# Optimization experiments

Measured on AMD Instinct MI355X. Metric: run time of the kernel, lower is better.

## Reference

```python
import jax, jax.numpy as jnp
import numpy as np

B, C, H, W = 2, 128, 64, 64
N, R = 16, 4            # d_state, dt_rank = ceil(128/32)
R2 = 2 * R
Ch = C // 2
Cout = 128
L = H * W
EPS_LN = 1e-6
EPS_BN = 1e-5


def _ln_cf(x, w, b):
    # channels_first LayerNorm over dim 1
    u = x.mean(1, keepdims=True)
    s = ((x - u) ** 2).mean(1, keepdims=True)
    return w[None, :, None, None] * (x - u) / jnp.sqrt(s + EPS_LN) + b[None, :, None, None]


def _conv1x1(x, w, b):
    return jnp.einsum('bchw,oc->bohw', x, w) + b[None, :, None, None]


def _dwconv(x, w, b):
    out = jax.lax.conv_general_dilated(x, w, (1, 1), 'SAME',
        dimension_numbers=('NCHW', 'OIHW', 'NCHW'), feature_group_count=x.shape[1])
    return out + b[None, :, None, None]


def _selective_scan(u, delta, A, Bs, Cs, D):
    # u, delta: [B,L,C]; A: [C,N]; Bs, Cs: [B,L,N]; D: [C]
    dA = jnp.exp(delta[..., None] * A)                   # [B,L,C,N]
    dBu = (delta * u)[..., None] * Bs[:, :, None, :]     # [B,L,C,N]
    def step(h, xs):
        a, b = xs
        h = a * h + b
        return h, h
    h0 = jnp.zeros((u.shape[0], u.shape[2], A.shape[1]), u.dtype)
    _, hs = jax.lax.scan(step, h0, (jnp.moveaxis(dA, 1, 0), jnp.moveaxis(dBu, 1, 0)))
    hs = jnp.moveaxis(hs, 0, 1)                          # [B,L,C,N]
    return jnp.einsum('blcn,bln->blc', hs, Cs) + u * D


def _branch_ssm(x, xp_w, xp_b, dt_w, dt_b, A_log, Dp, reverse):
    b_, c_, h_, w_ = x.shape
    u = x.reshape(b_, c_, -1).transpose(0, 2, 1)         # [B,L,C/2]
    if reverse:
        u = u[:, ::-1]
    dbl = u @ xp_w.T + xp_b
    dt, Bs, Cs = jnp.split(dbl, [R, R + N], axis=-1)
    delta = jax.nn.softplus(dt @ dt_w.T + dt_b)
    y = _selective_scan(u, delta, -jnp.exp(A_log), Bs, Cs, Dp)
    if reverse:
        y = y[:, ::-1]
    return y.transpose(0, 2, 1).reshape(b_, c_, h_, w_)


def _sid_ssm(x, sorted_idx, xp_w, xp_b, dt_w, dt_b, A_log, Dp):
    b_, c_, h_, w_ = x.shape
    u = x.reshape(b_, c_, -1).transpose(0, 2, 1)         # [B,L,C]
    u = jnp.take_along_axis(u, sorted_idx[:, :, None], axis=1)
    dbl = u @ xp_w.T + xp_b
    dt, Bs, Cs = jnp.split(dbl, [R2, R2 + N], axis=-1)
    delta = jax.nn.softplus(dt @ dt_w.T + dt_b)
    y = _selective_scan(u, delta, -jnp.exp(A_log), Bs, Cs, Dp)
    inv = jnp.argsort(sorted_idx, axis=1)                # inverse permutation
    y = jnp.take_along_axis(y, inv[:, :, None], axis=1)
    return y.transpose(0, 2, 1).reshape(b_, c_, h_, w_)


def _forward(x, mask_fg, mask_bg, mask_uc,
             norm_in_w, norm_in_b, in_proj_w, in_proj_b,
             ln_mamba_w, ln_mamba_b, conv_mamba_w, conv_mamba_b,
             conv_res_w, conv_res_b,
             xproj_f_w, xproj_f_b, dtproj_f_w, dtproj_f_b, A_log_f, D_f,
             xproj_b_w, xproj_b_b, dtproj_b_w, dtproj_b_b, A_log_b, D_b,
             xproj_s_w, xproj_s_b, dtproj_s_w, dtproj_s_b, A_log_s, D_s,
             ln_cat_w, ln_cat_b,
             g0_w, g0_b, bn_g, bn_be, bn_m, bn_v, g1_w, g1_b,
             out_w, out_b, norm_out_w, norm_out_b):
    x = _ln_cf(x, norm_in_w, norm_in_b)
    xp = _conv1x1(x, in_proj_w, in_proj_b)               # [B,2C,H,W]
    x_mamba, x_res = xp[:, :C], xp[:, C:]
    x_mamba = _ln_cf(x_mamba, ln_mamba_w, ln_mamba_b)
    x_mamba = jax.nn.silu(_dwconv(x_mamba, conv_mamba_w, conv_mamba_b))
    x_res = jax.nn.silu(_dwconv(x_res, conv_res_w, conv_res_b))
    xf, xb = x_mamba[:, :Ch], x_mamba[:, Ch:]
    y_f = _branch_ssm(xf, xproj_f_w, xproj_f_b, dtproj_f_w, dtproj_f_b, A_log_f, D_f, False)
    y_b = _branch_ssm(xb, xproj_b_w, xproj_b_b, dtproj_b_w, dtproj_b_b, A_log_b, D_b, True)
    concat = _ln_cf(jnp.concatenate([y_f, y_b], 1), ln_cat_w, ln_cat_b)
    # SID priority ordering: fg > bg > uc > rest, ties broken by raster index
    fg = (mask_fg > 0.5).astype(x.dtype)
    bg = (mask_bg > 0.5).astype(x.dtype) * (1 - fg)
    uc = (mask_uc > 0.5).astype(x.dtype) * (1 - fg) * (1 - bg)
    prio = (fg * 3 + bg * 2 + uc).reshape(x.shape[0], -1) \
        + jnp.arange(L, dtype=x.dtype)[None] * 1e-4
    sorted_idx = jnp.argsort(-prio, axis=1)
    sid = _sid_ssm(x_mamba, sorted_idx, xproj_s_w, xproj_s_b, dtproj_s_w, dtproj_s_b, A_log_s, D_s)
    # gated fusion (BatchNorm in eval mode with running stats)
    g = _conv1x1(jnp.concatenate([concat, sid], 1), g0_w, g0_b)
    g = (g - bn_m[None, :, None, None]) / jnp.sqrt(bn_v + EPS_BN)[None, :, None, None]
    g = jax.nn.relu(g * bn_g[None, :, None, None] + bn_be[None, :, None, None])
    g = jax.nn.sigmoid(_conv1x1(g, g1_w, g1_b))
    fused = g * sid + (1 - g) * concat
    out = _conv1x1(jnp.concatenate([fused, x_res], 1), out_w, out_b)
    return _ln_cf(out, norm_out_w, norm_out_b)


def setup_inputs():
    keys = iter(jax.random.split(jax.random.key(0), 64))
    def rn(shape, s=1.0):
        return jax.random.normal(next(keys), shape, jnp.float32) * s
    def dt_bias(ch):
        dt = jnp.exp(jax.random.uniform(next(keys), (ch,)) * (np.log(0.1) - np.log(0.001)) + np.log(0.001))
        return dt + jnp.log(-jnp.expm1(-dt))  # inverse-softplus init as in torch code
    def a_log(ch):
        return jnp.log(jnp.tile(jnp.arange(1, N + 1, dtype=jnp.float32), (ch, 1)))
    s = 0.05
    return dict(
        x=rn((B, C, H, W)),
        mask_fg=jax.random.uniform(next(keys), (B, 1, H, W)),
        mask_bg=jax.random.uniform(next(keys), (B, 1, H, W)),
        mask_uc=jax.random.uniform(next(keys), (B, 1, H, W)),
        norm_in_w=jnp.ones((C,)), norm_in_b=jnp.zeros((C,)),
        in_proj_w=rn((2 * C, C), s), in_proj_b=jnp.zeros((2 * C,)),
        ln_mamba_w=jnp.ones((C,)), ln_mamba_b=jnp.zeros((C,)),
        conv_mamba_w=rn((C, 1, 3, 3), 0.2), conv_mamba_b=jnp.zeros((C,)),
        conv_res_w=rn((C, 1, 3, 3), 0.2), conv_res_b=jnp.zeros((C,)),
        xproj_f_w=rn((R + 2 * N, Ch), s), xproj_f_b=jnp.zeros((R + 2 * N,)),
        dtproj_f_w=rn((Ch, R), 0.5), dtproj_f_b=dt_bias(Ch),
        A_log_f=a_log(Ch), D_f=jnp.ones((Ch,)),
        xproj_b_w=rn((R + 2 * N, Ch), s), xproj_b_b=jnp.zeros((R + 2 * N,)),
        dtproj_b_w=rn((Ch, R), 0.5), dtproj_b_b=dt_bias(Ch),
        A_log_b=a_log(Ch), D_b=jnp.ones((Ch,)),
        xproj_s_w=rn((R2 + 2 * N, C), s), xproj_s_b=jnp.zeros((R2 + 2 * N,)),
        dtproj_s_w=rn((C, R2), 0.35), dtproj_s_b=dt_bias(C),
        A_log_s=a_log(C), D_s=jnp.ones((C,)),
        ln_cat_w=jnp.ones((C,)), ln_cat_b=jnp.zeros((C,)),
        g0_w=rn((C, 2 * C), s), g0_b=jnp.zeros((C,)),
        bn_g=jnp.ones((C,)), bn_be=jnp.zeros((C,)),
        bn_m=jnp.zeros((C,)), bn_v=jnp.ones((C,)),
        g1_w=rn((C, C), s), g1_b=jnp.zeros((C,)),
        out_w=rn((Cout, 2 * C), s), out_b=jnp.zeros((Cout,)),
        norm_out_w=jnp.ones((Cout,)), norm_out_b=jnp.zeros((Cout,)),
    )


def reference(x, mask_fg, mask_bg, mask_uc,
              norm_in_w, norm_in_b, in_proj_w, in_proj_b,
              ln_mamba_w, ln_mamba_b, conv_mamba_w, conv_mamba_b,
              conv_res_w, conv_res_b,
              xproj_f_w, xproj_f_b, dtproj_f_w, dtproj_f_b, A_log_f, D_f,
              xproj_b_w, xproj_b_b, dtproj_b_w, dtproj_b_b, A_log_b, D_b,
              xproj_s_w, xproj_s_b, dtproj_s_w, dtproj_s_b, A_log_s, D_s,
              ln_cat_w, ln_cat_b,
              g0_w, g0_b, bn_g, bn_be, bn_m, bn_v, g1_w, g1_b,
              out_w, out_b, norm_out_w, norm_out_b):
    return _forward(x, mask_fg, mask_bg, mask_uc,
                    norm_in_w, norm_in_b, in_proj_w, in_proj_b,
                    ln_mamba_w, ln_mamba_b, conv_mamba_w, conv_mamba_b,
                    conv_res_w, conv_res_b,
                    xproj_f_w, xproj_f_b, dtproj_f_w, dtproj_f_b, A_log_f, D_f,
                    xproj_b_w, xproj_b_b, dtproj_b_w, dtproj_b_b, A_log_b, D_b,
                    xproj_s_w, xproj_s_b, dtproj_s_w, dtproj_s_b, A_log_s, D_s,
                    ln_cat_w, ln_cat_b,
                    g0_w, g0_b, bn_g, bn_be, bn_m, bn_v, g1_w, g1_b,
                    out_w, out_b, norm_out_w, norm_out_b)
```

## Files before the change

### kernel.cpp

```cpp
#include <hip/hip_runtime.h>
#include <math.h>

#define Bn 2
#define Cn_ 128
#define Hn 64
#define Wn 64
#define Ln 4096
#define Nn 16

static constexpr float EPS_LN_C = 1e-6f;
static constexpr float EPS_BN_C = 1e-5f;

__device__ __forceinline__ float softplusf_(float x) {
    return fmaxf(x, 0.f) + log1pf(__expf(-fabsf(x)));
}
__device__ __forceinline__ float sigmoidf_(float x) {
    return 1.f / (1.f + __expf(-x));
}

__global__ __launch_bounds__(256) void ln_kernel(
    const float* __restrict__ inA, const float* __restrict__ inB, int csA,
    const float* __restrict__ lw, const float* __restrict__ lb,
    float* __restrict__ out, int csOut) {
    int b = blockIdx.y;
// ... 101 lines not shown
        for (int j = 0; j < 4; j++) {
            int o = o0 + j;
            if (o >= cout) continue;
            float4 v = acc[j];
            if (epilogue == 1) {
                float sc = (1.f / sqrtf(bnv[o] + EPS_BN_C)) * bng[o];
                float sh = bnbe[o] - bnm[o] * sc;
                v.x = fmaxf(fmaf(v.x, sc, sh), 0.f);
                v.y = fmaxf(fmaf(v.y, sc, sh), 0.f);
                v.z = fmaxf(fmaf(v.z, sc, sh), 0.f);
                v.w = fmaxf(fmaf(v.w, sc, sh), 0.f);
            } else if (epilogue == 2) {
                v.x = sigmoidf_(v.x); v.y = sigmoidf_(v.y);
                v.z = sigmoidf_(v.z); v.w = sigmoidf_(v.w);
            }
            *(float4*)(out + ((size_t)b * csOut + o) * Ln + l) = v;
        }
    }
}

__global__ __launch_bounds__(256) void combine_kernel(
    const float* __restrict__ p0, const float* __restrict__ p1,
    const float* __restrict__ p2, const float* __restrict__ p3, int ksn,
    const float* __restrict__ bias,
    const float* __restrict__ bng, const float* __restrict__ bnbe,
    const float* __restrict__ bnm, const float* __restrict__ bnv,
    int epilogue, float* __restrict__ out, int cout, int n4) {
    int i = blockIdx.x * 256 + threadIdx.x;
    if (i >= n4) return;
    size_t e = (size_t)i * 4;
    int o = (int)((e / Ln) % cout);
    float4 a = *(const float4*)(p0 + e);
    if (ksn > 1) { float4 t = *(const float4*)(p1 + e); a.x += t.x; a.y += t.y; a.z += t.z; a.w += t.w; }
    if (ksn > 2) { float4 t = *(const float4*)(p2 + e); a.x += t.x; a.y += t.y; a.z += t.z; a.w += t.w; }
    if (ksn > 3) { float4 t = *(const float4*)(p3 + e); a.x += t.x; a.y += t.y; a.z += t.z; a.w += t.w; }
    float bj = bias[o];
    a.x += bj; a.y += bj; a.z += bj; a.w += bj;
    if (epilogue == 1) {
        float sc = (1.f / sqrtf(bnv[o] + EPS_BN_C)) * bng[o];
        float sh = bnbe[o] - bnm[o] * sc;
        a.x = fmaxf(fmaf(a.x, sc, sh), 0.f);
        a.y = fmaxf(fmaf(a.y, sc, sh), 0.f);
        a.z = fmaxf(fmaf(a.z, sc, sh), 0.f);
        a.w = fmaxf(fmaf(a.w, sc, sh), 0.f);
    } else if (epilogue == 2) {
        a.x = sigmoidf_(a.x); a.y = sigmoidf_(a.y);
        a.z = sigmoidf_(a.z); a.w = sigmoidf_(a.w);
    }
    *(float4*)(out + e) = a;
}

__global__ void dwconv_kernel(const float* __restrict__ xmn, const float* __restrict__ xp,
                              const float* __restrict__ wm, const float* __restrict__ bm,
                              const float* __restrict__ wr, const float* __restrict__ brr,
                              float* __restrict__ xm, float* __restrict__ xr) {
    int b = blockIdx.z;
    int c2 = blockIdx.y;
    int l = blockIdx.x * blockDim.x + threadIdx.x;
    int h = l >> 6, w = l & 63;
    bool mamba = (c2 < 128);
    const float* in = mamba ? (xmn + ((size_t)b * 128 + c2) * Ln)
                            : (xp + ((size_t)b * 256 + c2) * Ln);
    const float* wt = mamba ? (wm + c2 * 9) : (wr + (c2 - 128) * 9);
    float acc = mamba ? bm[c2] : brr[c2 - 128];
#pragma unroll
    for (int dh = -1; dh <= 1; dh++) {
#pragma unroll
        for (int dw = -1; dw <= 1; dw++) {
            int hh = h + dh, ww = w + dw;
            if (hh < 0 || hh > 63 || ww < 0 || ww > 63) continue;
            acc = fmaf(in[hh * 64 + ww], wt[(dh + 1) * 3 + (dw + 1)], acc);
        }
    }
    float o = acc * sigmoidf_(acc);
    if (mamba) xm[((size_t)b * 128 + c2) * Ln + l] = o;
    else       xr[((size_t)b * 128 + (c2 - 128)) * Ln + l] = o;
}

__global__ __launch_bounds__(1024) void sort_kernel(const float* __restrict__ mfg,
                                                    const float* __restrict__ mbg,
// ... 89 lines not shown
#pragma unroll
    for (int r = 0; r < R; r++) {
        float wv = dtw[c * R + r];
        acc.x = fmaf(wv, a[r].x, acc.x);
        acc.y = fmaf(wv, a[r].y, acc.y);
        acc.z = fmaf(wv, a[r].z, acc.z);
        acc.w = fmaf(wv, a[r].w, acc.w);
    }
    float4 o;
    o.x = softplusf_(acc.x); o.y = softplusf_(acc.y);
    o.z = softplusf_(acc.z); o.w = softplusf_(acc.w);
    *(float4*)(dpk + (((size_t)b * NQ + cq) * 1024 + tq) * 16 + clow * 4) = o;
}

__global__ __launch_bounds__(256) void pack_bc_kernel(
    const float* __restrict__ dblf, const float* __restrict__ dblb, const float* __restrict__ dbls,
    float* __restrict__ bf, float* __restrict__ cf,
    float* __restrict__ bb2, float* __restrict__ cb2,
    float* __restrict__ bs, float* __restrict__ cs) {
    int br = blockIdx.z;
    int b = blockIdx.y;
    int idx = blockIdx.x * 256 + threadIdx.x;
    int tb = idx >> 4, n = idx & 15;
    const float* src; float* dB; float* dC; int RT, rB, rC;
    if (br == 0)      { src = dblf; dB = bf;  dC = cf;  RT = 36; rB = 4; rC = 20; }
    else if (br == 1) { src = dblb; dB = bb2; dC = cb2; RT = 36; rB = 4; rC = 20; }
    else              { src = dbls; dB = bs;  dC = cs;  RT = 40; rB = 8; rC = 24; }
    float4 vB = *(const float4*)(src + ((size_t)b * RT + rB + n) * Ln + tb * 4);
    float4 vC = *(const float4*)(src + ((size_t)b * RT + rC + n) * Ln + tb * 4);
    *(float4*)(dB + ((size_t)b * 1024 + tb) * 64 + n * 4) = vB;
    *(float4*)(dC + ((size_t)b * 1024 + tb) * 64 + n * 4) = vC;
}

#define NCHUNK 64
#define CG 4

#define DPPADD(p) do { \
    p += __int_as_float(__builtin_amdgcn_update_dpp(0, __float_as_int(p), 0xB1, 0xF, 0xF, true)); \
    p += __int_as_float(__builtin_amdgcn_update_dpp(0, __float_as_int(p), 0x4E, 0xF, 0xF, true)); \
    p += __int_as_float(__builtin_amdgcn_update_dpp(0, __float_as_int(p), 0x124, 0xF, 0xF, true)); \
    p += __int_as_float(__builtin_amdgcn_update_dpp(0, __float_as_int(p), 0x128, 0xF, 0xF, true)); \
} while (0)

template <int REV>
__device__ __forceinline__ void p1_chunk(const float* __restrict__ up, const float* __restrict__ dp,
                                         const float* __restrict__ bp, float A, int c0,
                                         float& hout, float& Pout) {
    float h = 0.f, P = 1.f;
    float4 U0[4], D0[4], B0[4], U1[4], D1[4], B1[4];
#define PHYS1(ci) (REV ? (255 - (ci)) : (ci))
#define LOAD1(U, D, Bb, ci) do { int pb_ = PHYS1(ci) * 16; int tb_ = PHYS1(ci) * 4; \
    _Pragma("unroll") for (int j_ = 0; j_ < 4; ++j_) { \
        U[j_]  = *(const float4*)(up + pb_ + 4 * j_); \
        D[j_]  = *(const float4*)(dp + (size_t)(tb_ + j_) * 16); \
        Bb[j_] = *(const float4*)(bp + (size_t)(tb_ + j_) * 64); \
    } } while (0)
#define STEP1(u_, d_, B_) do { float a_ = __expf((d_) * A); h = fmaf(a_, h, (d_) * (u_) * (B_)); P *= a_; } while (0)
#define COMP1(U, D, Bb) do { \
    if (!REV) { _Pragma("unroll") for (int j_ = 0; j_ < 4; ++j_) { \
        STEP1(U[j_].x, D[j_].x, Bb[j_].x); STEP1(U[j_].y, D[j_].y, Bb[j_].y); \
        STEP1(U[j_].z, D[j_].z, Bb[j_].z); STEP1(U[j_].w, D[j_].w, Bb[j_].w); } } \
    else { _Pragma("unroll") for (int j_ = 3; j_ >= 0; --j_) { \
        STEP1(U[j_].w, D[j_].w, Bb[j_].w); STEP1(U[j_].z, D[j_].z, Bb[j_].z); \
        STEP1(U[j_].y, D[j_].y, Bb[j_].y); STEP1(U[j_].x, D[j_].x, Bb[j_].x); } } } while (0)
    LOAD1(U0, D0, B0, c0);
    for (int it = 0; it < CG; it += 2) {
        LOAD1(U1, D1, B1, c0 + it + 1);
        COMP1(U0, D0, B0);
        if (it + 2 < CG) LOAD1(U0, D0, B0, c0 + it + 2);
        COMP1(U1, D1, B1);
    }
    hout = h; Pout = P;
#undef PHYS1
#undef LOAD1
#undef STEP1
#undef COMP1
}

__global__ __launch_bounds__(256) void scan_p1_kernel(
    const float* __restrict__ xm, const float* __restrict__ us,
    const float* __restrict__ dfpk, const float* __restrict__ bpkf, const float* __restrict__ Alf,
    const float* __restrict__ dbpk, const float* __restrict__ bpkb, const float* __restrict__ Alb,
    const float* __restrict__ dspk, const float* __restrict__ bpks, const float* __restrict__ Als,
    float* __restrict__ hf, float* __restrict__ Pp) {
    int g = blockIdx.x * 4 + (threadIdx.x >> 6), k = blockIdx.y;
    int lane = threadIdx.x & 63;
    int n = lane & 15, cl = lane >> 4;
    int c0 = k * CG;
    float h, P;
    if (g < 32) {
        int b = g >> 4, cg = g & 15, c = cg * 4 + cl;
        float A = -__expf(Alf[c * 16 + n]);
        p1_chunk<0>(xm + ((size_t)b * 128 + c) * Ln,
                    dfpk + (((size_t)b * 16 + cg) * 1024) * 16 + cl * 4,
                    bpkf + (size_t)b * 65536 + n * 4, A, c0, h, P);
    } else if (g < 64) {
        int g2 = g - 32, b = g2 >> 4, cg = g2 & 15, c = cg * 4 + cl;
        float A = -__expf(Alb[c * 16 + n]);
        p1_chunk<1>(xm + ((size_t)b * 128 + 64 + c) * Ln,
                    dbpk + (((size_t)b * 16 + cg) * 1024) * 16 + cl * 4,
                    bpkb + (size_t)b * 65536 + n * 4, A, c0, h, P);
    } else {
        int g2 = g - 64, b = g2 >> 5, cg = g2 & 31, c = cg * 4 + cl;
        float A = -__expf(Als[c * 16 + n]);
        p1_chunk<0>(us + ((size_t)b * 128 + c) * Ln,
                    dspk + (((size_t)b * 32 + cg) * 1024) * 16 + cl * 4,
                    bpks + (size_t)b * 65536 + n * 4, A, c0, h, P);
    }
    int o = (g * NCHUNK + k) * 64 + lane;
    hf[o] = h; Pp[o] = P;
}

__global__ void scan_stitch_kernel(const float* __restrict__ hf, const float* __restrict__ Pp,
                                   float* __restrict__ hi) {
    int id = blockIdx.x * blockDim.x + threadIdx.x;
    int g = id >> 6, lane = id & 63;
    float h = 0.f;
    for (int kb = 0; kb < NCHUNK / 8; kb++) {
        float P8[8], H8[8];
#pragma unroll
        for (int j = 0; j < 8; j++) {
            int o = (g * NCHUNK + kb * 8 + j) * 64 + lane;
            P8[j] = Pp[o]; H8[j] = hf[o];
        }
#pragma unroll
        for (int j = 0; j < 8; j++) {
            int o = (g * NCHUNK + kb * 8 + j) * 64 + lane;
            hi[o] = h;
            h = fmaf(P8[j], h, H8[j]);
        }
    }
}

#define STEPP(u_, d_, B_, C_) ({ \
    float dA_ = __expf((d_) * A); \
    h = fmaf(dA_, h, (d_) * (u_) * (B_)); \
    float p_ = h * (C_); \
    DPPADD(p_); \
    fmaf((u_), Dc, p_); })

template <int MODE>
__device__ __forceinline__ void p2_chunk(const float* __restrict__ up, const float* __restrict__ dp,
                                         const float* __restrict__ bp, const float* __restrict__ cp,
                                         const int* __restrict__ sp, float* __restrict__ yp,
                                         float A, float Dc, int n, int c0, float h) {
    constexpr bool REV = (MODE == 1);
    constexpr bool SIDM = (MODE == 2);
    float4 U0[4], D0[4], B0[4], C0[4], U1[4], D1[4], B1[4], C1[4];
    int4 I0[4] = {}, I1[4] = {};
#define PHYS(ci) (REV ? (255 - (ci)) : (ci))
#define LOADC(U, D, Bb, Cc, I, ci) do { int pb_ = PHYS(ci) * 16; int tb_ = PHYS(ci) * 4; \
    _Pragma("unroll") for (int j_ = 0; j_ < 4; ++j_) { \
        U[j_]  = *(const float4*)(up + pb_ + 4 * j_); \
        D[j_]  = *(const float4*)(dp + (size_t)(tb_ + j_) * 16); \
        Bb[j_] = *(const float4*)(bp + (size_t)(tb_ + j_) * 64); \
        Cc[j_] = *(const float4*)(cp + (size_t)(tb_ + j_) * 64); \
        if (SIDM) I[j_] = *(const int4*)(sp + pb_ + 4 * j_); \
    } } while (0)
#define COMPC(U, D, Bb, Cc, I, ci) do { int pb_ = PHYS(ci) * 16; \
    if (SIDM) { \
        _Pragma("unroll") for (int j_ = 0; j_ < 4; ++j_) { \
            float y0_ = STEPP(U[j_].x, D[j_].x, Bb[j_].x, Cc[j_].x); if (n == 0) yp[I[j_].x] = y0_; \
            float y1_ = STEPP(U[j_].y, D[j_].y, Bb[j_].y, Cc[j_].y); if (n == 0) yp[I[j_].y] = y1_; \
            float y2_ = STEPP(U[j_].z, D[j_].z, Bb[j_].z, Cc[j_].z); if (n == 0) yp[I[j_].z] = y2_; \
            float y3_ = STEPP(U[j_].w, D[j_].w, Bb[j_].w, Cc[j_].w); if (n == 0) yp[I[j_].w] = y3_; \
        } \
    } else if (!REV) { \
        _Pragma("unroll") for (int j_ = 0; j_ < 4; ++j_) { \
            float4 y4_; \
            y4_.x = STEPP(U[j_].x, D[j_].x, Bb[j_].x, Cc[j_].x); \
            y4_.y = STEPP(U[j_].y, D[j_].y, Bb[j_].y, Cc[j_].y); \
            y4_.z = STEPP(U[j_].z, D[j_].z, Bb[j_].z, Cc[j_].z); \
            y4_.w = STEPP(U[j_].w, D[j_].w, Bb[j_].w, Cc[j_].w); \
            if (n == 0) *(float4*)(yp + pb_ + 4 * j_) = y4_; \
        } \
    } else { \
        _Pragma("unroll") for (int j_ = 3; j_ >= 0; --j_) { \
            float4 y4_; \
            y4_.w = STEPP(U[j_].w, D[j_].w, Bb[j_].w, Cc[j_].w); \
            y4_.z = STEPP(U[j_].z, D[j_].z, Bb[j_].z, Cc[j_].z); \
            y4_.y = STEPP(U[j_].y, D[j_].y, Bb[j_].y, Cc[j_].y); \
            y4_.x = STEPP(U[j_].x, D[j_].x, Bb[j_].x, Cc[j_].x); \
            if (n == 0) *(float4*)(yp + pb_ + 4 * j_) = y4_; \
        } \
    } } while (0)
    LOADC(U0, D0, B0, C0, I0, c0);
    for (int it = 0; it < CG; it += 2) {
        LOADC(U1, D1, B1, C1, I1, c0 + it + 1);
        COMPC(U0, D0, B0, C0, I0, c0 + it);
        if (it + 2 < CG) LOADC(U0, D0, B0, C0, I0, c0 + it + 2);
        COMPC(U1, D1, B1, C1, I1, c0 + it + 1);
    }
#undef PHYS
#undef LOADC
#undef COMPC
}

__global__ __launch_bounds__(256) void scan_p2_kernel(
    const float* __restrict__ xm, const float* __restrict__ us,
    const float* __restrict__ dfpk, const float* __restrict__ bpkf, const float* __restrict__ cpkf,
    const float* __restrict__ Alf, const float* __restrict__ Dfp,
    const float* __restrict__ dbpk, const float* __restrict__ bpkb, const float* __restrict__ cpkb,
    const float* __restrict__ Alb, const float* __restrict__ Dbp,
    const float* __restrict__ dspk, const float* __restrict__ bpks, const float* __restrict__ cpks,
    const float* __restrict__ Als, const float* __restrict__ Dsp,
    const int* __restrict__ sidx, const float* __restrict__ hi,
    float* __restrict__ yf, float* __restrict__ yb, float* __restrict__ ys) {
    int g = blockIdx.x * 4 + (threadIdx.x >> 6), k = blockIdx.y;
    int lane = threadIdx.x & 63;
    int n = lane & 15, cl = lane >> 4;
    int c0 = k * CG;
    float h0 = hi[(g * NCHUNK + k) * 64 + lane];
    if (g < 32) {
        int b = g >> 4, cg = g & 15, c = cg * 4 + cl;
        float A = -__expf(Alf[c * 16 + n]);
        p2_chunk<0>(xm + ((size_t)b * 128 + c) * Ln,
                    dfpk + (((size_t)b * 16 + cg) * 1024) * 16 + cl * 4,
                    bpkf + (size_t)b * 65536 + n * 4, cpkf + (size_t)b * 65536 + n * 4,
                    nullptr, yf + ((size_t)b * 64 + c) * Ln, A, Dfp[c], n, c0, h0);
    } else if (g < 64) {
        int g2 = g - 32, b = g2 >> 4, cg = g2 & 15, c = cg * 4 + cl;
        float A = -__expf(Alb[c * 16 + n]);
        p2_chunk<1>(xm + ((size_t)b * 128 + 64 + c) * Ln,
                    dbpk + (((size_t)b * 16 + cg) * 1024) * 16 + cl * 4,
                    bpkb + (size_t)b * 65536 + n * 4, cpkb + (size_t)b * 65536 + n * 4,
                    nullptr, yb + ((size_t)b * 64 + c) * Ln, A, Dbp[c], n, c0, h0);
    } else {
        int g2 = g - 64, b = g2 >> 5, cg = g2 & 31, c = cg * 4 + cl;
        float A = -__expf(Als[c * 16 + n]);
        p2_chunk<2>(us + ((size_t)b * 128 + c) * Ln,
                    dspk + (((size_t)b * 32 + cg) * 1024) * 16 + cl * 4,
                    bpks + (size_t)b * 65536 + n * 4, cpks + (size_t)b * 65536 + n * 4,
                    sidx + b * Ln, ys + ((size_t)b * 128 + c) * Ln, A, Dsp[c], n, c0, h0);
    }
}

__global__ void fuse_kernel(const float4* __restrict__ gate, const float4* __restrict__ ysb,
                            const float4* __restrict__ cat, float4* __restrict__ out, int n4) {
    int i = blockIdx.x * blockDim.x + threadIdx.x;
    if (i < n4) {
        float4 g = gate[i], s = ysb[i], c = cat[i], o;
        o.x = g.x * s.x + (1.f - g.x) * c.x;
        o.y = g.y * s.y + (1.f - g.y) * c.y;
        o.z = g.z * s.z + (1.f - g.z) * c.z;
        o.w = g.w * s.w + (1.f - g.w) * c.w;
        out[i] = o;
    }
}

extern "C" void kernel_launch(void* const* d_in, const int* in_sizes, int n_in,
                              void* d_out, int out_size, void* d_ws, size_t ws_size,
                              hipStream_t stream) {
    const float* x    = (const float*)d_in[0];
    const float* mfg  = (const float*)d_in[1];
    const float* mbg  = (const float*)d_in[2];
    const float* muc  = (const float*)d_in[3];
    const float* niw  = (const float*)d_in[4];
    const float* nib  = (const float*)d_in[5];
    const float* inw  = (const float*)d_in[6];
    const float* inb  = (const float*)d_in[7];
    const float* lmw  = (const float*)d_in[8];
    const float* lmb  = (const float*)d_in[9];
    const float* cmw  = (const float*)d_in[10];
    const float* cmb  = (const float*)d_in[11];
    const float* crw  = (const float*)d_in[12];
    const float* crb  = (const float*)d_in[13];
    const float* xwf  = (const float*)d_in[14];
    const float* xbf  = (const float*)d_in[15];
    const float* dtwf = (const float*)d_in[16];
    const float* dtbf = (const float*)d_in[17];
    const float* Alf  = (const float*)d_in[18];
    const float* Dfp  = (const float*)d_in[19];
    const float* xwb  = (const float*)d_in[20];
    const float* xbb  = (const float*)d_in[21];
    const float* dtwb = (const float*)d_in[22];
    const float* dtbb = (const float*)d_in[23];
    const float* Alb  = (const float*)d_in[24];
    const float* Dbp  = (const float*)d_in[25];
    const float* xws  = (const float*)d_in[26];
// ... 3 lines not shown
    const float* Als  = (const float*)d_in[30];
    const float* Dsp  = (const float*)d_in[31];
    const float* lcw  = (const float*)d_in[32];
    const float* lcb  = (const float*)d_in[33];
    const float* g0w  = (const float*)d_in[34];
    const float* g0b  = (const float*)d_in[35];
    const float* bng  = (const float*)d_in[36];
    const float* bnbe = (const float*)d_in[37];
    const float* bnm  = (const float*)d_in[38];
    const float* bnv  = (const float*)d_in[39];
    const float* g1w  = (const float*)d_in[40];
    const float* g1b  = (const float*)d_in[41];
    const float* outw = (const float*)d_in[42];
    const float* outb = (const float*)d_in[43];
    const float* now  = (const float*)d_in[44];
    const float* nob  = (const float*)d_in[45];

    float* W = (float*)d_ws;
    const size_t R_XP = 0;
    const size_t R_A  = 2097152;
    const size_t R_B  = 4194304;
    const size_t R_N  = 6291456;
    const size_t R_XM = 7340032;
    const size_t R_XR = 8388608;
    const size_t R_US = 9437184;
    const size_t R_IDX= 10485760;
    const size_t XNORM = R_N, XP = R_XP, XMN = R_N;
    const size_t XPJ0 = R_XP, XPJ1 = R_XP + 294912;
    const size_t DBLF = R_B, DBLB = R_B + 294912, DBLS = R_B + 589824;
    const size_t DFPK = R_N, DBPK = R_N + 524288, DSPK = R_B + 1048576;
    const size_t BPKF = R_A, CPKF = R_A + 131072, BPKB = R_A + 262144,
                 CPKB = R_A + 393216, BPKS = R_A + 524288, CPKS = R_A + 655360;
    const size_t XS0 = R_XP, XS1 = R_XP + 327680, XS2 = R_XP + 655360, XS3 = R_XP + 983040;
    const size_t HF = R_XP, PP = R_XP + 524288, HI = R_XP + 1048576;
    const size_t YF = R_A + 786432, YB = R_A + 1310720, YS = R_B;
    const size_t CATLN = R_N, FUSED = R_N;
    const size_t GBUF = R_XM, GATE = R_US, OUTB = R_US;

    int* idxp = (int*)(W + R_IDX);
    dim3 blk(256);
    const float* nil = nullptr;

    ln_kernel<<<dim3(64, 2), blk, 0, stream>>>(x, nullptr, 128, niw, nib, W + XNORM, 128);
    conv1x1_kernel<<<dim3(4, 128, 2), blk, 0, stream>>>(
        W + XNORM, nullptr, 128, 128, 0, 0, 256, 256, inw, nullptr, inb, nullptr, 0,
        nil, nil, nil, nil, 0, nullptr, 2, 64, W + R_A, W + R_B, nullptr, nullptr, 0);
    combine_kernel<<<2048, blk, 0, stream>>>(
        W + R_A, W + R_B, nullptr, nullptr, 2, inb, nil, nil, nil, nil, 0, W + XP, 256, 524288);
    ln_kernel<<<dim3(64, 2), blk, 0, stream>>>(W + XP, nullptr, 256, lmw, lmb, W + XMN, 128);
    dwconv_kernel<<<dim3(16, 256, 2), blk, 0, stream>>>(
        W + XMN, W + XP, cmw, cmb, crw, crb, W + R_XM, W + R_XR);
    sort_kernel<<<2, 1024, 0, stream>>>(mfg, mbg, muc, idxp);
    conv1x1_kernel<<<dim3(4, 18, 4), blk, 0, stream>>>(
        W + R_XM, nullptr, 64, 128, 0, 0, 36, 36, xwf, xwb, xbf, xbb, (long)64 * Ln,
        nil, nil, nil, nil, 0, nullptr, 2, 32, W + XPJ0, W + XPJ1, nullptr, nullptr, (long)589824);
    combine_kernel<<<288, blk, 0, stream>>>(
        W + XPJ0, W + XPJ1, nullptr, nullptr, 2, xbf, nil, nil, nil, nil, 0, W + DBLF, 36, 73728);
    combine_kernel<<<288, blk, 0, stream>>>(
        W + XPJ0 + 589824, W + XPJ1 + 589824, nullptr, nullptr, 2, xbb,
        nil, nil, nil, nil, 0, W + DBLB, 36, 73728);
    delta_pack_kernel<4, 16><<<dim3(16, 16, 2), blk, 0, stream>>>(W + DBLF, 36, dtwf, dtbf, W + DFPK);
    delta_pack_kernel<4, 16><<<dim3(16, 16, 2), blk, 0, stream>>>(W + DBLB, 36, dtwb, dtbb, W + DBPK);
    gather_kernel<<<dim3(16, 128, 2), blk, 0, stream>>>(W + R_XM, idxp, W + R_US);
    conv1x1_kernel<<<dim3(4, 40, 2), blk, 0, stream>>>(
        W + R_US, nullptr, 128, 128, 0, 0, 40, 40, xws, nullptr, xbs, nullptr, 0,
        nil, nil, nil, nil, 0, nullptr, 4, 32, W + XS0, W + XS1, W + XS2, W + XS3, 0);
    combine_kernel<<<320, blk, 0, stream>>>(
        W + XS0, W + XS1, W + XS2, W + XS3, 4, xbs, nil, nil, nil, nil, 0, W + DBLS, 40, 81920);
    pack_bc_kernel<<<dim3(64, 2, 3), blk, 0, stream>>>(
        W + DBLF, W + DBLB, W + DBLS,
        W + BPKF, W + CPKF, W + BPKB, W + CPKB, W + BPKS, W + CPKS);
    delta_pack_kernel<8, 32><<<dim3(16, 32, 2), blk, 0, stream>>>(W + DBLS, 40, dtws, dtbs, W + DSPK);
    scan_p1_kernel<<<dim3(32, NCHUNK), blk, 0, stream>>>(
        W + R_XM, W + R_US,
        W + DFPK, W + BPKF, Alf,
        W + DBPK, W + BPKB, Alb,
        W + DSPK, W + BPKS, Als,
        W + HF, W + PP);
    scan_stitch_kernel<<<32, 256, 0, stream>>>(W + HF, W + PP, W + HI);
    scan_p2_kernel<<<dim3(32, NCHUNK), blk, 0, stream>>>(
        W + R_XM, W + R_US,
        W + DFPK, W + BPKF, W + CPKF, Alf, Dfp,
        W + DBPK, W + BPKB, W + CPKB, Alb, Dbp,
        W + DSPK, W + BPKS, W + CPKS, Als, Dsp,
        idxp, W + HI, W + YF, W + YB, W + YS);
    ln_kernel<<<dim3(64, 2), blk, 0, stream>>>(W + YF, W + YB, 64, lcw, lcb, W + CATLN, 128);
    conv1x1_kernel<<<dim3(4, 128, 2), blk, 0, stream>>>(
        W + CATLN, W + YS, 128, 128, 128, 128, 128, 128, g0w, nullptr, g0b, nullptr, 0,
        nil, nil, nil, nil, 0, nullptr, 4, 64,
        W + R_A, W + R_A + 1048576, W + R_XP, W + R_XP + 1048576, 0);
    combine_kernel<<<1024, blk, 0, stream>>>(
        W + R_A, W + R_A + 1048576, W + R_XP, W + R_XP + 1048576, 4, g0b,
        bng, bnbe, bnm, bnv, 1, W + GBUF, 128, 262144);
    conv1x1_kernel<<<dim3(4, 64, 2), blk, 0, stream>>>(
        W + GBUF, nullptr, 128, 128, 0, 0, 128, 128, g1w, nullptr, g1b, nullptr, 0,
        nil, nil, nil, nil, 0, nullptr, 2, 64, W + R_A, W + R_A + 1048576, nullptr, nullptr, 0);
    combine_kernel<<<1024, blk, 0, stream>>>(
        W + R_A, W + R_A + 1048576, nullptr, nullptr, 2, g1b,
        nil, nil, nil, nil, 2, W + GATE, 128, 262144);
    fuse_kernel<<<1024, blk, 0, stream>>>(
        (const float4*)(W + GATE), (const float4*)(W + YS), (const float4*)(W + CATLN),
        (float4*)(W + FUSED), Bn * Cn_ * Ln / 4);
    conv1x1_kernel<<<dim3(4, 128, 2), blk, 0, stream>>>(
        W + FUSED, W + R_XR, 128, 128, 128, 128, 128, 128, outw, nullptr, outb, nullptr, 0,
        nil, nil, nil, nil, 0, nullptr, 4, 64,
        W + R_A, W + R_A + 1048576, W + R_XP, W + R_XP + 1048576, 0);
    combine_kernel<<<1024, blk, 0, stream>>>(
        W + R_A, W + R_A + 1048576, W + R_XP, W + R_XP + 1048576, 4, outb,
        nil, nil, nil, nil, 0, W + OUTB, 128, 262144);
    ln_kernel<<<dim3(64, 2), blk, 0, stream>>>(W + OUTB, nullptr, 128, now, nob,
                                               (float*)d_out, 128);
}
```

Before: 232.9 us.

## Halve scan chunk count, deepen load prefetch, launch one-wave blocks

The chunked selective-scan kernels now use 32 chunks instead of 64, so each chunk covers 128 timesteps, loaded as 16 batches of 8 through a 4-slot rotating register buffer with 3-batch lookahead. The earlier scheme double-buffered 4 groups of 16 steps. Blocks shrink to a single 64-thread wavefront, and the workspace offsets for the per-chunk state buffers are resized to match. The aim is better memory-latency hiding and a cheaper stitch pass. The cost is half as many wavefronts available in parallel and longer sequential work per thread.

```diff
diff --git a/kernel.cpp b/kernel.cpp
--- a/kernel.cpp
+++ b/kernel.cpp
@@ -326,8 +326,7 @@
     *(float4*)(dC + ((size_t)b * 1024 + tb) * 64 + n * 4) = vC;
 }
 
-#define NCHUNK 64
-#define CG 4
+#define NCHUNK 32
 
 #define DPPADD(p) do { \
     p += __int_as_float(__builtin_amdgcn_update_dpp(0, __float_as_int(p), 0xB1, 0xF, 0xF, true)); \
@@ -338,68 +337,71 @@
 
 template <int REV>
 __device__ __forceinline__ void p1_chunk(const float* __restrict__ up, const float* __restrict__ dp,
-                                         const float* __restrict__ bp, float A, int c0,
+                                         const float* __restrict__ bp, float A, int k,
                                          float& hout, float& Pout) {
     float h = 0.f, P = 1.f;
-    float4 U0[4], D0[4], B0[4], U1[4], D1[4], B1[4];
-#define PHYS1(ci) (REV ? (255 - (ci)) : (ci))
-#define LOAD1(U, D, Bb, ci) do { int pb_ = PHYS1(ci) * 16; int tb_ = PHYS1(ci) * 4; \
-    _Pragma("unroll") for (int j_ = 0; j_ < 4; ++j_) { \
-        U[j_]  = *(const float4*)(up + pb_ + 4 * j_); \
-        D[j_]  = *(const float4*)(dp + (size_t)(tb_ + j_) * 16); \
-        Bb[j_] = *(const float4*)(bp + (size_t)(tb_ + j_) * 64); \
-    } } while (0)
-#define STEP1(u_, d_, B_) do { float a_ = __expf((d_) * A); h = fmaf(a_, h, (d_) * (u_) * (B_)); P *= a_; } while (0)
-#define COMP1(U, D, Bb) do { \
-    if (!REV) { _Pragma("unroll") for (int j_ = 0; j_ < 4; ++j_) { \
-        STEP1(U[j_].x, D[j_].x, Bb[j_].x); STEP1(U[j_].y, D[j_].y, Bb[j_].y); \
-        STEP1(U[j_].z, D[j_].z, Bb[j_].z); STEP1(U[j_].w, D[j_].w, Bb[j_].w); } } \
-    else { _Pragma("unroll") for (int j_ = 3; j_ >= 0; --j_) { \
-        STEP1(U[j_].w, D[j_].w, Bb[j_].w); STEP1(U[j_].z, D[j_].z, Bb[j_].z); \
-        STEP1(U[j_].y, D[j_].y, Bb[j_].y); STEP1(U[j_].x, D[j_].x, Bb[j_].x); } } } while (0)
-    LOAD1(U0, D0, B0, c0);
-    for (int it = 0; it < CG; it += 2) {
-        LOAD1(U1, D1, B1, c0 + it + 1);
-        COMP1(U0, D0, B0);
-        if (it + 2 < CG) LOAD1(U0, D0, B0, c0 + it + 2);
-        COMP1(U1, D1, B1);
+    float4 U[4][2], D[4][2], Bv[4][2];
+#define E1(bt) (REV ? (511 - (k * 16 + (bt))) : (k * 16 + (bt)))
+#define LB1(s) do { int e_ = E1(s); int bi_ = (s) & 3; \
+    U[bi_][0]  = *(const float4*)(up + e_ * 8); \
+    U[bi_][1]  = *(const float4*)(up + e_ * 8 + 4); \
+    D[bi_][0]  = *(const float4*)(dp + (size_t)(e_ * 2) * 16); \
+    D[bi_][1]  = *(const float4*)(dp + (size_t)(e_ * 2 + 1) * 16); \
+    Bv[bi_][0] = *(const float4*)(bp + (size_t)(e_ * 2) * 64); \
+    Bv[bi_][1] = *(const float4*)(bp + (size_t)(e_ * 2 + 1) * 64); } while (0)
+#define ST1(u_, d_, B_) do { float a_ = __expf((d_) * A); h = fmaf(a_, h, (d_) * (u_) * (B_)); P *= a_; } while (0)
+#define CB1(s) do { int bi_ = (s) & 3; \
+    if (!REV) { _Pragma("unroll") for (int j_ = 0; j_ < 2; ++j_) { \
+        ST1(U[bi_][j_].x, D[bi_][j_].x, Bv[bi_][j_].x); \
+        ST1(U[bi_][j_].y, D[bi_][j_].y, Bv[bi_][j_].y); \
+        ST1(U[bi_][j_].z, D[bi_][j_].z, Bv[bi_][j_].z); \
+        ST1(U[bi_][j_].w, D[bi_][j_].w, Bv[bi_][j_].w); } } \
+    else { _Pragma("unroll") for (int j_ = 1; j_ >= 0; --j_) { \
+        ST1(U[bi_][j_].w, D[bi_][j_].w, Bv[bi_][j_].w); \
+        ST1(U[bi_][j_].z, D[bi_][j_].z, Bv[bi_][j_].z); \
+        ST1(U[bi_][j_].y, D[bi_][j_].y, Bv[bi_][j_].y); \
+        ST1(U[bi_][j_].x, D[bi_][j_].x, Bv[bi_][j_].x); } } } while (0)
+    LB1(0); LB1(1); LB1(2);
+#pragma unroll
+    for (int bt = 0; bt < 16; ++bt) {
+        if (bt + 3 < 16) LB1(bt + 3);
+        CB1(bt);
     }
     hout = h; Pout = P;
-#undef PHYS1
-#undef LOAD1
-#undef STEP1
-#undef COMP1
-}
-
-__global__ __launch_bounds__(256) void scan_p1_kernel(
+#undef E1
+#undef LB1
+#undef ST1
+#undef CB1
+}
+
+__global__ __launch_bounds__(64) void scan_p1_kernel(
     const float* __restrict__ xm, const float* __restrict__ us,
     const float* __restrict__ dfpk, const float* __restrict__ bpkf, const float* __restrict__ Alf,
     const float* __restrict__ dbpk, const float* __restrict__ bpkb, const float* __restrict__ Alb,
     const float* __restrict__ dspk, const float* __restrict__ bpks, const float* __restrict__ Als,
     float* __restrict__ hf, float* __restrict__ Pp) {
-    int g = blockIdx.x * 4 + (threadIdx.x >> 6), k = blockIdx.y;
-    int lane = threadIdx.x & 63;
+    int g = blockIdx.x, k = blockIdx.y;
+    int lane = threadIdx.x;
     int n = lane & 15, cl = lane >> 4;
-    int c0 = k * CG;
     float h, P;
     if (g < 32) {
         int b = g >> 4, cg = g & 15, c = cg * 4 + cl;
         float A = -__expf(Alf[c * 16 + n]);
         p1_chunk<0>(xm + ((size_t)b * 128 + c) * Ln,
                     dfpk + (((size_t)b * 16 + cg) * 1024) * 16 + cl * 4,
-                    bpkf + (size_t)b * 65536 + n * 4, A, c0, h, P);
+                    bpkf + (size_t)b * 65536 + n * 4, A, k, h, P);
     } else if (g < 64) {
         int g2 = g - 32, b = g2 >> 4, cg = g2 & 15, c = cg * 4 + cl;
         float A = -__expf(Alb[c * 16 + n]);
         p1_chunk<1>(xm + ((size_t)b * 128 + 64 + c) * Ln,
                     dbpk + (((size_t)b * 16 + cg) * 1024) * 16 + cl * 4,
-                    bpkb + (size_t)b * 65536 + n * 4, A, c0, h, P);
+                    bpkb + (size_t)b * 65536 + n * 4, A, k, h, P);
     } else {
         int g2 = g - 64, b = g2 >> 5, cg = g2 & 31, c = cg * 4 + cl;
         float A = -__expf(Als[c * 16 + n]);
         p1_chunk<0>(us + ((size_t)b * 128 + c) * Ln,
                     dspk + (((size_t)b * 32 + cg) * 1024) * 16 + cl * 4,
-                    bpks + (size_t)b * 65536 + n * 4, A, c0, h, P);
+                    bpks + (size_t)b * 65536 + n * 4, A, k, h, P);
     }
     int o = (g * NCHUNK + k) * 64 + lane;
     hf[o] = h; Pp[o] = P;
@@ -437,60 +439,62 @@
 __device__ __forceinline__ void p2_chunk(const float* __restrict__ up, const float* __restrict__ dp,
                                          const float* __restrict__ bp, const float* __restrict__ cp,
                                          const int* __restrict__ sp, float* __restrict__ yp,
-                                         float A, float Dc, int n, int c0, float h) {
+                                         float A, float Dc, int n, int k, float h) {
     constexpr bool REV = (MODE == 1);
     constexpr bool SIDM = (MODE == 2);
-    float4 U0[4], D0[4], B0[4], C0[4], U1[4], D1[4], B1[4], C1[4];
-    int4 I0[4] = {}, I1[4] = {};
-#define PHYS(ci) (REV ? (255 - (ci)) : (ci))
-#define LOADC(U, D, Bb, Cc, I, ci) do { int pb_ = PHYS(ci) * 16; int tb_ = PHYS(ci) * 4; \
-    _Pragma("unroll") for (int j_ = 0; j_ < 4; ++j_) { \
-        U[j_]  = *(const float4*)(up + pb_ + 4 * j_); \
-        D[j_]  = *(const float4*)(dp + (size_t)(tb_ + j_) * 16); \
-        Bb[j_] = *(const float4*)(bp + (size_t)(tb_ + j_) * 64); \
-        Cc[j_] = *(const float4*)(cp + (size_t)(tb_ + j_) * 64); \
-        if (SIDM) I[j_] = *(const int4*)(sp + pb_ + 4 * j_); \
-    } } while (0)
-#define COMPC(U, D, Bb, Cc, I, ci) do { int pb_ = PHYS(ci) * 16; \
+    float4 U[4][2], D[4][2], Bv[4][2], Cv[4][2];
+    int4 I[4][2] = {};
+#define E2(bt) (REV ? (511 - (k * 16 + (bt))) : (k * 16 + (bt)))
+#define LB2(s) do { int e_ = E2(s); int bi_ = (s) & 3; \
+    U[bi_][0]  = *(const float4*)(up + e_ * 8); \
+    U[bi_][1]  = *(const float4*)(up + e_ * 8 + 4); \
+    D[bi_][0]  = *(const float4*)(dp + (size_t)(e_ * 2) * 16); \
+    D[bi_][1]  = *(const float4*)(dp + (size_t)(e_ * 2 + 1) * 16); \
+    Bv[bi_][0] = *(const float4*)(bp + (size_t)(e_ * 2) * 64); \
+    Bv[bi_][1] = *(const float4*)(bp + (size_t)(e_ * 2 + 1) * 64); \
+    Cv[bi_][0] = *(const float4*)(cp + (size_t)(e_ * 2) * 64); \
+    Cv[bi_][1] = *(const float4*)(cp + (size_t)(e_ * 2 + 1) * 64); \
+    if (SIDM) { I[bi_][0] = *(const int4*)(sp + e_ * 8); \
+                I[bi_][1] = *(const int4*)(sp + e_ * 8 + 4); } } while (0)
+#define CB2(s) do { int e_ = E2(s); int bi_ = (s) & 3; \
     if (SIDM) { \
-        _Pragma("unroll") for (int j_ = 0; j_ < 4; ++j_) { \
-            float y0_ = STEPP(U[j_].x, D[j_].x, Bb[j_].x, Cc[j_].x); if (n == 0) yp[I[j_].x] = y0_; \
-            float y1_ = STEPP(U[j_].y, D[j_].y, Bb[j_].y, Cc[j_].y); if (n == 0) yp[I[j_].y] = y1_; \
-            float y2_ = STEPP(U[j_].z, D[j_].z, Bb[j_].z, Cc[j_].z); if (n == 0) yp[I[j_].z] = y2_; \
-            float y3_ = STEPP(U[j_].w, D[j_].w, Bb[j_].w, Cc[j_].w); if (n == 0) yp[I[j_].w] = y3_; \
+        _Pragma("unroll") for (int j_ = 0; j_ < 2; ++j_) { \
+            float y0_ = STEPP(U[bi_][j_].x, D[bi_][j_].x, Bv[bi_][j_].x, Cv[bi_][j_].x); if (n == 0) yp[I[bi_][j_].x] = y0_; \
+            float y1_ = STEPP(U[bi_][j_].y, D[bi_][j_].y, Bv[bi_][j_].y, Cv[bi_][j_].y); if (n == 0) yp[I[bi_][j_].y] = y1_; \
+            float y2_ = STEPP(U[bi_][j_].z, D[bi_][j_].z, Bv[bi_][j_].z, Cv[bi_][j_].z); if (n == 0) yp[I[bi_][j_].z] = y2_; \
+            float y3_ = STEPP(U[bi_][j_].w, D[bi_][j_].w, Bv[bi_][j_].w, Cv[bi_][j_].w); if (n == 0) yp[I[bi_][j_].w] = y3_; \
         } \
     } else if (!REV) { \
-        _Pragma("unroll") for (int j_ = 0; j_ < 4; ++j_) { \
+        _Pragma("unroll") for (int j_ = 0; j_ < 2; ++j_) { \
             float4 y4_; \
-            y4_.x = STEPP(U[j_].x, D[j_].x, Bb[j_].x, Cc[j_].x); \
-            y4_.y = STEPP(U[j_].y, D[j_].y, Bb[j_].y, Cc[j_].y); \
-            y4_.z = STEPP(U[j_].z, D[j_].z, Bb[j_].z, Cc[j_].z); \
-            y4_.w = STEPP(U[j_].w, D[j_].w, Bb[j_].w, Cc[j_].w); \
-            if (n == 0) *(float4*)(yp + pb_ + 4 * j_) = y4_; \
+            y4_.x = STEPP(U[bi_][j_].x, D[bi_][j_].x, Bv[bi_][j_].x, Cv[bi_][j_].x); \
+            y4_.y = STEPP(U[bi_][j_].y, D[bi_][j_].y, Bv[bi_][j_].y, Cv[bi_][j_].y); \
+            y4_.z = STEPP(U[bi_][j_].z, D[bi_][j_].z, Bv[bi_][j_].z, Cv[bi_][j_].z); \
+            y4_.w = STEPP(U[bi_][j_].w, D[bi_][j_].w, Bv[bi_][j_].w, Cv[bi_][j_].w); \
+            if (n == 0) *(float4*)(yp + e_ * 8 + 4 * j_) = y4_; \
         } \
     } else { \
-        _Pragma("unroll") for (int j_ = 3; j_ >= 0; --j_) { \
+        _Pragma("unroll") for (int j_ = 1; j_ >= 0; --j_) { \
             float4 y4_; \
-            y4_.w = STEPP(U[j_].w, D[j_].w, Bb[j_].w, Cc[j_].w); \
-            y4_.z = STEPP(U[j_].z, D[j_].z, Bb[j_].z, Cc[j_].z); \
-            y4_.y = STEPP(U[j_].y, D[j_].y, Bb[j_].y, Cc[j_].y); \
-            y4_.x = STEPP(U[j_].x, D[j_].x, Bb[j_].x, Cc[j_].x); \
-            if (n == 0) *(float4*)(yp + pb_ + 4 * j_) = y4_; \
+            y4_.w = STEPP(U[bi_][j_].w, D[bi_][j_].w, Bv[bi_][j_].w, Cv[bi_][j_].w); \
+            y4_.z = STEPP(U[bi_][j_].z, D[bi_][j_].z, Bv[bi_][j_].z, Cv[bi_][j_].z); \
+            y4_.y = STEPP(U[bi_][j_].y, D[bi_][j_].y, Bv[bi_][j_].y, Cv[bi_][j_].y); \
+            y4_.x = STEPP(U[bi_][j_].x, D[bi_][j_].x, Bv[bi_][j_].x, Cv[bi_][j_].x); \
+            if (n == 0) *(float4*)(yp + e_ * 8 + 4 * j_) = y4_; \
         } \
     } } while (0)
-    LOADC(U0, D0, B0, C0, I0, c0);
-    for (int it = 0; it < CG; it += 2) {
-        LOADC(U1, D1, B1, C1, I1, c0 + it + 1);
-        COMPC(U0, D0, B0, C0, I0, c0 + it);
-        if (it + 2 < CG) LOADC(U0, D0, B0, C0, I0, c0 + it + 2);
-        COMPC(U1, D1, B1, C1, I1, c0 + it + 1);
-    }
-#undef PHYS
-#undef LOADC
-#undef COMPC
-}
-
-__global__ __launch_bounds__(256) void scan_p2_kernel(
+    LB2(0); LB2(1); LB2(2);
+#pragma unroll
+    for (int bt = 0; bt < 16; ++bt) {
+        if (bt + 3 < 16) LB2(bt + 3);
+        CB2(bt);
+    }
+#undef E2
+#undef LB2
+#undef CB2
+}
+
+__global__ __launch_bounds__(64) void scan_p2_kernel(
     const float* __restrict__ xm, const float* __restrict__ us,
     const float* __restrict__ dfpk, const float* __restrict__ bpkf, const float* __restrict__ cpkf,
     const float* __restrict__ Alf, const float* __restrict__ Dfp,
@@ -500,10 +504,9 @@
     const float* __restrict__ Als, const float* __restrict__ Dsp,
     const int* __restrict__ sidx, const float* __restrict__ hi,
     float* __restrict__ yf, float* __restrict__ yb, float* __restrict__ ys) {
-    int g = blockIdx.x * 4 + (threadIdx.x >> 6), k = blockIdx.y;
-    int lane = threadIdx.x & 63;
+    int g = blockIdx.x, k = blockIdx.y;
+    int lane = threadIdx.x;
     int n = lane & 15, cl = lane >> 4;
-    int c0 = k * CG;
     float h0 = hi[(g * NCHUNK + k) * 64 + lane];
     if (g < 32) {
         int b = g >> 4, cg = g & 15, c = cg * 4 + cl;
@@ -511,21 +514,21 @@
         p2_chunk<0>(xm + ((size_t)b * 128 + c) * Ln,
                     dfpk + (((size_t)b * 16 + cg) * 1024) * 16 + cl * 4,
                     bpkf + (size_t)b * 65536 + n * 4, cpkf + (size_t)b * 65536 + n * 4,
-                    nullptr, yf + ((size_t)b * 64 + c) * Ln, A, Dfp[c], n, c0, h0);
+                    nullptr, yf + ((size_t)b * 64 + c) * Ln, A, Dfp[c], n, k, h0);
     } else if (g < 64) {
         int g2 = g - 32, b = g2 >> 4, cg = g2 & 15, c = cg * 4 + cl;
         float A = -__expf(Alb[c * 16 + n]);
         p2_chunk<1>(xm + ((size_t)b * 128 + 64 + c) * Ln,
                     dbpk + (((size_t)b * 16 + cg) * 1024) * 16 + cl * 4,
                     bpkb + (size_t)b * 65536 + n * 4, cpkb + (size_t)b * 65536 + n * 4,
-                    nullptr, yb + ((size_t)b * 64 + c) * Ln, A, Dbp[c], n, c0, h0);
+                    nullptr, yb + ((size_t)b * 64 + c) * Ln, A, Dbp[c], n, k, h0);
     } else {
         int g2 = g - 64, b = g2 >> 5, cg = g2 & 31, c = cg * 4 + cl;
         float A = -__expf(Als[c * 16 + n]);
         p2_chunk<2>(us + ((size_t)b * 128 + c) * Ln,
                     dspk + (((size_t)b * 32 + cg) * 1024) * 16 + cl * 4,
                     bpks + (size_t)b * 65536 + n * 4, cpks + (size_t)b * 65536 + n * 4,
-                    sidx + b * Ln, ys + ((size_t)b * 128 + c) * Ln, A, Dsp[c], n, c0, h0);
+                    sidx + b * Ln, ys + ((size_t)b * 128 + c) * Ln, A, Dsp[c], n, k, h0);
     }
 }
 
@@ -608,7 +611,7 @@
     const size_t BPKF = R_A, CPKF = R_A + 131072, BPKB = R_A + 262144,
                  CPKB = R_A + 393216, BPKS = R_A + 524288, CPKS = R_A + 655360;
     const size_t XS0 = R_XP, XS1 = R_XP + 327680, XS2 = R_XP + 655360, XS3 = R_XP + 983040;
-    const size_t HF = R_XP, PP = R_XP + 524288, HI = R_XP + 1048576;
+    const size_t HF = R_XP, PP = R_XP + 262144, HI = R_XP + 524288;
     const size_t YF = R_A + 786432, YB = R_A + 1310720, YS = R_B;
     const size_t CATLN = R_N, FUSED = R_N;
     const size_t GBUF = R_XM, GATE = R_US, OUTB = R_US;
@@ -647,14 +650,14 @@
         W + DBLF, W + DBLB, W + DBLS,
         W + BPKF, W + CPKF, W + BPKB, W + CPKB, W + BPKS, W + CPKS);
     delta_pack_kernel<8, 32><<<dim3(16, 32, 2), blk, 0, stream>>>(W + DBLS, 40, dtws, dtbs, W + DSPK);
-    scan_p1_kernel<<<dim3(32, NCHUNK), blk, 0, stream>>>(
+    scan_p1_kernel<<<dim3(128, NCHUNK), 64, 0, stream>>>(
         W + R_XM, W + R_US,
         W + DFPK, W + BPKF, Alf,
         W + DBPK, W + BPKB, Alb,
         W + DSPK, W + BPKS, Als,
         W + HF, W + PP);
     scan_stitch_kernel<<<32, 256, 0, stream>>>(W + HF, W + PP, W + HI);
-    scan_p2_kernel<<<dim3(32, NCHUNK), blk, 0, stream>>>(
+    scan_p2_kernel<<<dim3(128, NCHUNK), 64, 0, stream>>>(
         W + R_XM, W + R_US,
         W + DFPK, W + BPKF, W + CPKF, Alf, Dfp,
         W + DBPK, W + BPKB, W + CPKB, Alb, Dbp,
```

Result: slower. 280.9 us (+20.6%).

## Double scan chunk count, use single-wave blocks, fuse gating blend into combine

Applied to the files above, without the earlier changes.

The chunked selective scan now uses 128 chunks of 2 groups instead of 64 chunks of 4, and launches one 64-thread wave per block instead of four waves per block. This puts more independent work in flight during the latency-bound scan phases, at the cost of a longer stitch pass and more chunk-state traffic. The stitch kernel now writes its prefix states in place into the chunk-state buffer, which drops a separate buffer. The sigmoid-gate blend that fuse_kernel did is folded into the combine epilogue, removing one kernel launch and one full read and write of the gate tensor.

```diff
diff --git a/kernel.cpp b/kernel.cpp
--- a/kernel.cpp
+++ b/kernel.cpp
@@ -157,8 +157,10 @@
     int o = (int)((e / Ln) % cout);
     float4 a = *(const float4*)(p0 + e);
     if (ksn > 1) { float4 t = *(const float4*)(p1 + e); a.x += t.x; a.y += t.y; a.z += t.z; a.w += t.w; }
-    if (ksn > 2) { float4 t = *(const float4*)(p2 + e); a.x += t.x; a.y += t.y; a.z += t.z; a.w += t.w; }
-    if (ksn > 3) { float4 t = *(const float4*)(p3 + e); a.x += t.x; a.y += t.y; a.z += t.z; a.w += t.w; }
+    if (epilogue != 3) {
+        if (ksn > 2) { float4 t = *(const float4*)(p2 + e); a.x += t.x; a.y += t.y; a.z += t.z; a.w += t.w; }
+        if (ksn > 3) { float4 t = *(const float4*)(p3 + e); a.x += t.x; a.y += t.y; a.z += t.z; a.w += t.w; }
+    }
     float bj = bias[o];
     a.x += bj; a.y += bj; a.z += bj; a.w += bj;
     if (epilogue == 1) {
@@ -171,6 +173,14 @@
     } else if (epilogue == 2) {
         a.x = sigmoidf_(a.x); a.y = sigmoidf_(a.y);
         a.z = sigmoidf_(a.z); a.w = sigmoidf_(a.w);
+    } else if (epilogue == 3) {
+        float4 s = *(const float4*)(p2 + e);
+        float4 c = *(const float4*)(p3 + e);
+        float g;
+        g = sigmoidf_(a.x); a.x = g * s.x + (1.f - g) * c.x;
+        g = sigmoidf_(a.y); a.y = g * s.y + (1.f - g) * c.y;
+        g = sigmoidf_(a.z); a.z = g * s.z + (1.f - g) * c.z;
+        g = sigmoidf_(a.w); a.w = g * s.w + (1.f - g) * c.w;
     }
     *(float4*)(out + e) = a;
 }
@@ -326,8 +336,8 @@
     *(float4*)(dC + ((size_t)b * 1024 + tb) * 64 + n * 4) = vC;
 }
 
-#define NCHUNK 64
-#define CG 4
+#define NCHUNK 128
+#define CG 2
 
 #define DPPADD(p) do { \
     p += __int_as_float(__builtin_amdgcn_update_dpp(0, __float_as_int(p), 0xB1, 0xF, 0xF, true)); \
@@ -371,14 +381,14 @@
 #undef COMP1
 }
 
-__global__ __launch_bounds__(256) void scan_p1_kernel(
+__global__ __launch_bounds__(64) void scan_p1_kernel(
     const float* __restrict__ xm, const float* __restrict__ us,
     const float* __restrict__ dfpk, const float* __restrict__ bpkf, const float* __restrict__ Alf,
     const float* __restrict__ dbpk, const float* __restrict__ bpkb, const float* __restrict__ Alb,
     const float* __restrict__ dspk, const float* __restrict__ bpks, const float* __restrict__ Als,
     float* __restrict__ hf, float* __restrict__ Pp) {
-    int g = blockIdx.x * 4 + (threadIdx.x >> 6), k = blockIdx.y;
-    int lane = threadIdx.x & 63;
+    int g = blockIdx.x, k = blockIdx.y;
+    int lane = threadIdx.x;
     int n = lane & 15, cl = lane >> 4;
     int c0 = k * CG;
     float h, P;
@@ -405,8 +415,7 @@
     hf[o] = h; Pp[o] = P;
 }
 
-__global__ void scan_stitch_kernel(const float* __restrict__ hf, const float* __restrict__ Pp,
-                                   float* __restrict__ hi) {
+__global__ void scan_stitch_kernel(float* __restrict__ hf, const float* __restrict__ Pp) {
     int id = blockIdx.x * blockDim.x + threadIdx.x;
     int g = id >> 6, lane = id & 63;
     float h = 0.f;
@@ -420,7 +429,7 @@
 #pragma unroll
         for (int j = 0; j < 8; j++) {
             int o = (g * NCHUNK + kb * 8 + j) * 64 + lane;
-            hi[o] = h;
+            hf[o] = h;
             h = fmaf(P8[j], h, H8[j]);
         }
     }
@@ -490,7 +499,7 @@
 #undef COMPC
 }
 
-__global__ __launch_bounds__(256) void scan_p2_kernel(
+__global__ __launch_bounds__(64) void scan_p2_kernel(
     const float* __restrict__ xm, const float* __restrict__ us,
     const float* __restrict__ dfpk, const float* __restrict__ bpkf, const float* __restrict__ cpkf,
     const float* __restrict__ Alf, const float* __restrict__ Dfp,
@@ -500,8 +509,8 @@
     const float* __restrict__ Als, const float* __restrict__ Dsp,
     const int* __restrict__ sidx, const float* __restrict__ hi,
     float* __restrict__ yf, float* __restrict__ yb, float* __restrict__ ys) {
-    int g = blockIdx.x * 4 + (threadIdx.x >> 6), k = blockIdx.y;
-    int lane = threadIdx.x & 63;
+    int g = blockIdx.x, k = blockIdx.y;
+    int lane = threadIdx.x;
     int n = lane & 15, cl = lane >> 4;
     int c0 = k * CG;
     float h0 = hi[(g * NCHUNK + k) * 64 + lane];
@@ -526,19 +535,6 @@
                     dspk + (((size_t)b * 32 + cg) * 1024) * 16 + cl * 4,
                     bpks + (size_t)b * 65536 + n * 4, cpks + (size_t)b * 65536 + n * 4,
                     sidx + b * Ln, ys + ((size_t)b * 128 + c) * Ln, A, Dsp[c], n, c0, h0);
-    }
-}
-
-__global__ void fuse_kernel(const float4* __restrict__ gate, const float4* __restrict__ ysb,
-                            const float4* __restrict__ cat, float4* __restrict__ out, int n4) {
-    int i = blockIdx.x * blockDim.x + threadIdx.x;
-    if (i < n4) {
-        float4 g = gate[i], s = ysb[i], c = cat[i], o;
-        o.x = g.x * s.x + (1.f - g.x) * c.x;
-        o.y = g.y * s.y + (1.f - g.y) * c.y;
-        o.z = g.z * s.z + (1.f - g.z) * c.z;
-        o.w = g.w * s.w + (1.f - g.w) * c.w;
-        out[i] = o;
     }
 }
 
@@ -608,10 +604,10 @@
     const size_t BPKF = R_A, CPKF = R_A + 131072, BPKB = R_A + 262144,
                  CPKB = R_A + 393216, BPKS = R_A + 524288, CPKS = R_A + 655360;
     const size_t XS0 = R_XP, XS1 = R_XP + 327680, XS2 = R_XP + 655360, XS3 = R_XP + 983040;
-    const size_t HF = R_XP, PP = R_XP + 524288, HI = R_XP + 1048576;
+    const size_t HF = R_XP, PP = R_XP + 1048576;
     const size_t YF = R_A + 786432, YB = R_A + 1310720, YS = R_B;
     const size_t CATLN = R_N, FUSED = R_N;
-    const size_t GBUF = R_XM, GATE = R_US, OUTB = R_US;
+    const size_t GBUF = R_XM, OUTB = R_US;
 
     int* idxp = (int*)(W + R_IDX);
     dim3 blk(256);
@@ -647,19 +643,19 @@
         W + DBLF, W + DBLB, W + DBLS,
         W + BPKF, W + CPKF, W + BPKB, W + CPKB, W + BPKS, W + CPKS);
     delta_pack_kernel<8, 32><<<dim3(16, 32, 2), blk, 0, stream>>>(W + DBLS, 40, dtws, dtbs, W + DSPK);
-    scan_p1_kernel<<<dim3(32, NCHUNK), blk, 0, stream>>>(
+    scan_p1_kernel<<<dim3(128, NCHUNK), 64, 0, stream>>>(
         W + R_XM, W + R_US,
         W + DFPK, W + BPKF, Alf,
         W + DBPK, W + BPKB, Alb,
         W + DSPK, W + BPKS, Als,
         W + HF, W + PP);
-    scan_stitch_kernel<<<32, 256, 0, stream>>>(W + HF, W + PP, W + HI);
-    scan_p2_kernel<<<dim3(32, NCHUNK), blk, 0, stream>>>(
+    scan_stitch_kernel<<<32, 256, 0, stream>>>(W + HF, W + PP);
+    scan_p2_kernel<<<dim3(128, NCHUNK), 64, 0, stream>>>(
         W + R_XM, W + R_US,
         W + DFPK, W + BPKF, W + CPKF, Alf, Dfp,
         W + DBPK, W + BPKB, W + CPKB, Alb, Dbp,
         W + DSPK, W + BPKS, W + CPKS, Als, Dsp,
-        idxp, W + HI, W + YF, W + YB, W + YS);
+        idxp, W + HF, W + YF, W + YB, W + YS);
     ln_kernel<<<dim3(64, 2), blk, 0, stream>>>(W + YF, W + YB, 64, lcw, lcb, W + CATLN, 128);
     conv1x1_kernel<<<dim3(4, 128, 2), blk, 0, stream>>>(
         W + CATLN, W + YS, 128, 128, 128, 128, 128, 128, g0w, nullptr, g0b, nullptr, 0,
@@ -672,11 +668,8 @@
         W + GBUF, nullptr, 128, 128, 0, 0, 128, 128, g1w, nullptr, g1b, nullptr, 0,
         nil, nil, nil, nil, 0, nullptr, 2, 64, W + R_A, W + R_A + 1048576, nullptr, nullptr, 0);
     combine_kernel<<<1024, blk, 0, stream>>>(
-        W + R_A, W + R_A + 1048576, nullptr, nullptr, 2, g1b,
-        nil, nil, nil, nil, 2, W + GATE, 128, 262144);
-    fuse_kernel<<<1024, blk, 0, stream>>>(
-        (const float4*)(W + GATE), (const float4*)(W + YS), (const float4*)(W + CATLN),
-        (float4*)(W + FUSED), Bn * Cn_ * Ln / 4);
+        W + R_A, W + R_A + 1048576, W + YS, W + CATLN, 2, g1b,
+        nil, nil, nil, nil, 3, W + FUSED, 128, 262144);
     conv1x1_kernel<<<dim3(4, 128, 2), blk, 0, stream>>>(
         W + FUSED, W + R_XR, 128, 128, 128, 128, 128, 128, outw, nullptr, outb, nullptr, 0,
         nil, nil, nil, nil, 0, nullptr, 4, 64,
```

Result: faster. 223.8 us (-3.9%).
